# Performance work log

Hardware: AMD Instinct MI355X
Metric: run time of the kernel (lower is better)

## Reference

```python
import jax, jax.numpy as jnp
import numpy as np

HIDDEN = 2048
N_HEADS = 16
Q_DIM = N_HEADS * 128  # 2048
INTER = 10944
EPS = 1e-6
B, S = 2, 2048


def rms_norm(x, w, eps):
    var = jnp.mean(jnp.square(x), axis=-1, keepdims=True)
    return x * jax.lax.rsqrt(var + eps) * w


def setup_inputs() -> dict:
    key = jax.random.key(0)
    ks = jax.random.split(key, 8)
    x = jax.random.normal(ks[0], (B, S, HIDDEN), dtype=jnp.float32)
    positions = jnp.broadcast_to(jnp.arange(S, dtype=jnp.int32), (B, S))
    sc = 0.02
    return {
        "x": x,
        "positions": positions,
        "in_w": jnp.ones((HIDDEN,), dtype=jnp.float32),
        "post_w": jnp.ones((HIDDEN,), dtype=jnp.float32),
        "Wq": jax.random.normal(ks[1], (Q_DIM, HIDDEN), dtype=jnp.float32) * sc,
        "Wo": jax.random.normal(ks[2], (HIDDEN, Q_DIM), dtype=jnp.float32) * sc,
        "Wg": jax.random.normal(ks[3], (INTER, HIDDEN), dtype=jnp.float32) * sc,
        "Wu": jax.random.normal(ks[4], (INTER, HIDDEN), dtype=jnp.float32) * sc,
        "Wd": jax.random.normal(ks[5], (HIDDEN, INTER), dtype=jnp.float32) * sc,
    }


def reference(x, positions, in_w, post_w, Wq, Wo, Wg, Wu, Wd):
    b, s, h = x.shape
    xf = x.reshape(-1, h)                       # [T, H]
    h_norm = rms_norm(xf, in_w, EPS)            # RMSNorm (input_layernorm)
    q = jnp.einsum('th,qh->tq', h_norm, Wq)     # q_proj
    hidden = xf + jnp.einsum('tq,hq->th', q, Wo)  # o_proj + residual
    h_post = rms_norm(hidden, post_w, EPS)      # post_attention_layernorm
    gate = jax.nn.silu(jnp.einsum('th,ih->ti', h_post, Wg))
    up = jnp.einsum('th,ih->ti', h_post, Wu)
    mlp = jnp.einsum('ti,hi->th', gate * up, Wd)  # down_proj
    return (hidden + mlp).reshape(b, s, h)
```

## Files before the change

### kernel.cpp

```cpp
#include <hip/hip_runtime.h>
#include <hip/hip_bf16.h>
#include <stdint.h>


typedef __bf16 bf16;
typedef bf16 bf16x8 __attribute__((ext_vector_type(8)));
typedef bf16 bf16x4 __attribute__((ext_vector_type(4)));
typedef float f32x4 __attribute__((ext_vector_type(4)));

#define HID     2048
#define TOK     4096
#define INTER   10944
#define INTER_P 11008
#define BK      32

__device__ __forceinline__ void gload_lds16(const bf16* g, bf16* l) {
    __builtin_amdgcn_global_load_lds(
        (const __attribute__((address_space(1))) void*)g,
        (__attribute__((address_space(3))) void*)l, 16, 0, 0);
}

__global__ __launch_bounds__(256) void conv_pad(const float* __restrict__ src,
                                                bf16* __restrict__ dst,
                                                int n_src, int n_dst) {
    int i = (blockIdx.x * 256 + threadIdx.x) * 4;
    if (i >= n_dst) return;
    float4 v = make_float4(0.f, 0.f, 0.f, 0.f);
    if (i < n_src) v = *(const float4*)(src + i);
    bf16x4 o;
    o[0] = (bf16)v.x; o[1] = (bf16)v.y; o[2] = (bf16)v.z; o[3] = (bf16)v.w;
    *(bf16x4*)(dst + i) = o;
}

__global__ __launch_bounds__(256) void conv_wd(const float* __restrict__ src,
                                               bf16* __restrict__ dst) {
    int i = (blockIdx.x * 256 + threadIdx.x) * 4;
    if (i >= HID * INTER_P) return;
    int row = i / INTER_P;
    int col = i - row * INTER_P;
    float4 v = make_float4(0.f, 0.f, 0.f, 0.f);
    if (col < INTER)
        v = *(const float4*)(src + (size_t)row * INTER + col);
    bf16x4 o;
    o[0] = (bf16)v.x; o[1] = (bf16)v.y; o[2] = (bf16)v.z; o[3] = (bf16)v.w;
    *(bf16x4*)(dst + i) = o;
}

__global__ __launch_bounds__(256) void rmsnorm_k(const float* __restrict__ x,
                                                 const float* __restrict__ w,
                                                 bf16* __restrict__ out) {
    const int row = blockIdx.x;
    const int tid = threadIdx.x;
    const float* xr = x + (size_t)row * HID + tid * 8;
    float4 v0 = *(const float4*)(xr);
    float4 v1 = *(const float4*)(xr + 4);
    float s = v0.x * v0.x + v0.y * v0.y + v0.z * v0.z + v0.w * v0.w +
              v1.x * v1.x + v1.y * v1.y + v1.z * v1.z + v1.w * v1.w;
    #pragma unroll
    for (int o = 32; o > 0; o >>= 1) s += __shfl_down(s, o);
    __shared__ float red[4];
    if ((tid & 63) == 0) red[tid >> 6] = s;
    __syncthreads();
    float tot = red[0] + red[1] + red[2] + red[3];
    float scale = rsqrtf(tot * (1.0f / (float)HID) + 1e-6f);
    float4 w0 = *(const float4*)(w + tid * 8);
    float4 w1 = *(const float4*)(w + tid * 8 + 4);
    bf16x8 o8;
    o8[0] = (bf16)(v0.x * scale * w0.x);
    o8[1] = (bf16)(v0.y * scale * w0.y);
    o8[2] = (bf16)(v0.z * scale * w0.z);
    o8[3] = (bf16)(v0.w * scale * w0.w);
    o8[4] = (bf16)(v1.x * scale * w1.x);
    o8[5] = (bf16)(v1.y * scale * w1.y);
    o8[6] = (bf16)(v1.z * scale * w1.z);
    o8[7] = (bf16)(v1.w * scale * w1.w);
    *(bf16x8*)(out + (size_t)row * HID + tid * 8) = o8;
}

template <int EPI>
__global__ __launch_bounds__(512, 4) void gemm_bt5(const bf16* __restrict__ A,
                                                   const bf16* __restrict__ W,
                                                   const float* __restrict__ res,
                                                   void* __restrict__ out,
                                                   int N, int K) {
    __shared__ bf16 lA[128 * BK];
    __shared__ bf16 lW[128 * BK];
    const int tid = threadIdx.x;
    const int rowBase = blockIdx.x * 128;
    const int colBase = blockIdx.y * 128;
    const int wave = tid >> 6, lane = tid & 63;
    const int wm = (wave >> 2) * 64, wn = (wave & 3) * 32;
    const int lr = lane & 15, kq = lane >> 4;

    f32x4 acc[4][2] = {};
    const bf16* Ab = A + (size_t)rowBase * K;
    const bf16* Wb = W + (size_t)colBase * K;

    const int sr = tid >> 2;
    const int ss = (tid & 3) ^ ((sr >> 1) & 3);
    const size_t goff = (size_t)sr * K + ss * 8;

    int aoff[4], woff[2];
    #pragma unroll
    for (int i = 0; i < 4; ++i) {
        int r = wm + i * 16 + lr;
        aoff[i] = r * BK + (kq ^ ((r >> 1) & 3)) * 8;
    }
    #pragma unroll
    for (int i = 0; i < 2; ++i) {
        int r = wn + i * 16 + lr;
        woff[i] = r * BK + (kq ^ ((r >> 1) & 3)) * 8;
    }

    for (int k0 = 0; k0 < K; k0 += BK) {
        gload_lds16(Ab + goff + k0, &lA[tid * 8]);
        gload_lds16(Wb + goff + k0, &lW[tid * 8]);
        __syncthreads();
        bf16x8 af[4], wf[2];
        #pragma unroll
        for (int i = 0; i < 4; ++i) af[i] = *(const bf16x8*)&lA[aoff[i]];
        #pragma unroll
        for (int i = 0; i < 2; ++i) wf[i] = *(const bf16x8*)&lW[woff[i]];
        #pragma unroll
        for (int mi = 0; mi < 4; ++mi)
            #pragma unroll
            for (int ni = 0; ni < 2; ++ni)
                acc[mi][ni] = __builtin_amdgcn_mfma_f32_16x16x32_bf16(
                    af[mi], wf[ni], acc[mi][ni], 0, 0, 0);
        __syncthreads();
    }
    const int rq = lane >> 4, cn = lane & 15;
    #pragma unroll
    for (int mi = 0; mi < 4; ++mi) {
        #pragma unroll
        for (int ni = 0; ni < 2; ++ni) {
            int col = colBase + wn + ni * 16 + cn;
            #pragma unroll
            for (int r = 0; r < 4; ++r) {
                int row = rowBase + wm + mi * 16 + rq * 4 + r;
                size_t idx = (size_t)row * N + col;
                float v = acc[mi][ni][r];
                if (EPI == 0) ((bf16*)out)[idx] = (bf16)v;
                else          ((float*)out)[idx] = res[idx] + v;
            }
        }
    }
}

__global__ __launch_bounds__(512, 4) void gemm_gu5(const bf16* __restrict__ A,
                                                   const bf16* __restrict__ Wg,
                                                   const bf16* __restrict__ Wu,
                                                   bf16* __restrict__ out,
                                                   int N, int K) {
    __shared__ bf16 lA[128 * BK];
    __shared__ bf16 lG[128 * BK];
    __shared__ bf16 lU[128 * BK];
    const int tid = threadIdx.x;
    const int rowBase = blockIdx.x * 128;
    const int colBase = blockIdx.y * 128;
    const int wave = tid >> 6, lane = tid & 63;
    const int wm = (wave >> 2) * 64, wn = (wave & 3) * 32;
    const int lr = lane & 15, kq = lane >> 4;

    f32x4 ag[4][2] = {};
    f32x4 au[4][2] = {};
    const bf16* Ab = A + (size_t)rowBase * K;
    const bf16* Gb = Wg + (size_t)colBase * K;
    const bf16* Ub = Wu + (size_t)colBase * K;

    const int sr = tid >> 2;
    const int ss = (tid & 3) ^ ((sr >> 1) & 3);
    const size_t goff = (size_t)sr * K + ss * 8;

    int aoff[4], boff[2];
    #pragma unroll
    for (int i = 0; i < 4; ++i) {
        int r = wm + i * 16 + lr;
        aoff[i] = r * BK + (kq ^ ((r >> 1) & 3)) * 8;
    }
    #pragma unroll
    for (int i = 0; i < 2; ++i) {
        int r = wn + i * 16 + lr;
        boff[i] = r * BK + (kq ^ ((r >> 1) & 3)) * 8;
    }

    for (int k0 = 0; k0 < K; k0 += BK) {
        gload_lds16(Ab + goff + k0, &lA[tid * 8]);
        gload_lds16(Gb + goff + k0, &lG[tid * 8]);
        gload_lds16(Ub + goff + k0, &lU[tid * 8]);
        __syncthreads();
        bf16x8 af[4], gf[2], uf[2];
        #pragma unroll
        for (int i = 0; i < 4; ++i) af[i] = *(const bf16x8*)&lA[aoff[i]];
        #pragma unroll
        for (int i = 0; i < 2; ++i) {
            gf[i] = *(const bf16x8*)&lG[boff[i]];
            uf[i] = *(const bf16x8*)&lU[boff[i]];
        }
        #pragma unroll
        for (int mi = 0; mi < 4; ++mi)
            #pragma unroll
            for (int ni = 0; ni < 2; ++ni) {
                ag[mi][ni] = __builtin_amdgcn_mfma_f32_16x16x32_bf16(
                    af[mi], gf[ni], ag[mi][ni], 0, 0, 0);
                au[mi][ni] = __builtin_amdgcn_mfma_f32_16x16x32_bf16(
                    af[mi], uf[ni], au[mi][ni], 0, 0, 0);
            }
        __syncthreads();
    }
    const int rq = lane >> 4, cn = lane & 15;
    #pragma unroll
    for (int mi = 0; mi < 4; ++mi) {
        #pragma unroll
        for (int ni = 0; ni < 2; ++ni) {
            int col = colBase + wn + ni * 16 + cn;
            #pragma unroll
            for (int r = 0; r < 4; ++r) {
                int row = rowBase + wm + mi * 16 + rq * 4 + r;
                float g = ag[mi][ni][r];
                float u = au[mi][ni][r];
                float sg = g / (1.0f + __expf(-g));
                out[(size_t)row * N + col] = (bf16)(sg * u);
            }
        }
    }
}

extern "C" void kernel_launch(void* const* d_in, const int* in_sizes, int n_in,
                              void* d_out, int out_size, void* d_ws, size_t ws_size,
                              hipStream_t stream) {
    const float* x      = (const float*)d_in[0];
    const float* in_w   = (const float*)d_in[2];
    const float* post_w = (const float*)d_in[3];
    const float* Wq     = (const float*)d_in[4];
    const float* Wo     = (const float*)d_in[5];
    const float* Wg     = (const float*)d_in[6];
    const float* Wu     = (const float*)d_in[7];
    const float* Wd     = (const float*)d_in[8];

    char* ws = (char*)d_ws;
    bf16*  X    = (bf16*)(ws + 0);
    bf16*  Yq   = (bf16*)(ws + 16777216);
    float* hid  = (float*)(ws + 33554432);
    bf16*  gu   = (bf16*)(ws + 67108864);
    bf16*  w0   = (bf16*)(ws + 157286400);
    bf16*  w1   = (bf16*)(ws + 202375168);
    bf16*  wsm  = (bf16*)(ws + 247463936);

    const int nGU  = INTER_P * HID;
    const int nGUs = INTER * HID;
    const int nSq  = HID * HID;

    conv_pad<<<nGU / 4 / 256, 256, 0, stream>>>(Wg, w0, nGUs, nGU);
    conv_pad<<<nGU / 4 / 256, 256, 0, stream>>>(Wu, w1, nGUs, nGU);
    conv_pad<<<nSq / 4 / 256, 256, 0, stream>>>(Wq, wsm, nSq, nSq);

    rmsnorm_k<<<TOK, 256, 0, stream>>>(x, in_w, X);
    gemm_bt5<0><<<dim3(TOK / 128, HID / 128), 512, 0, stream>>>(
        X, wsm, nullptr, Yq, HID, HID);
    conv_pad<<<nSq / 4 / 256, 256, 0, stream>>>(Wo, wsm, nSq, nSq);
    gemm_bt5<1><<<dim3(TOK / 128, HID / 128), 512, 0, stream>>>(
        Yq, wsm, x, hid, HID, HID);
    rmsnorm_k<<<TOK, 256, 0, stream>>>(hid, post_w, X);
    gemm_gu5<<<dim3(TOK / 128, INTER_P / 128), 512, 0, stream>>>(
        X, w0, w1, gu, INTER_P, HID);
    conv_wd<<<nGU / 4 / 256, 256, 0, stream>>>(Wd, w0);
    gemm_bt5<1><<<dim3(TOK / 128, HID / 128), 512, 0, stream>>>(
        gu, w0, hid, (float*)d_out, HID, INTER_P);
}
```

Baseline: 1.093 ms.

## Rewrite GEMMs with 256x128 tiles and multi-stage async LDS pipelining

Replaces the single-buffered 128x128 GEMM kernels with 256-row tiles whose K loop runs through a 3-stage (projections/down) or 4-stage (gate/up) ring of LDS buffers. Global-to-LDS loads for future K steps are interleaved between MFMA phases, with vmcnt waits, raw barriers and setprio hints. The goal is to hide global memory latency and raise arithmetic intensity per block. In exchange it uses much more LDS and registers per block, which lowers occupancy, and the hand-written barrier and waitcnt scheme is fragile.

```diff
diff --git a/kernel.cpp b/kernel.cpp
--- a/kernel.cpp
+++ b/kernel.cpp
@@ -12,13 +12,16 @@
 #define TOK     4096
 #define INTER   10944
 #define INTER_P 11008
-#define BK      32
 
 __device__ __forceinline__ void gload_lds16(const bf16* g, bf16* l) {
     __builtin_amdgcn_global_load_lds(
         (const __attribute__((address_space(1))) void*)g,
         (__attribute__((address_space(3))) void*)l, 16, 0, 0);
 }
+
+#define SBAR()      asm volatile("s_barrier" ::: "memory")
+#define WAIT_BAR(n) asm volatile("s_waitcnt vmcnt(" #n ")\n\ts_barrier" ::: "memory")
+#define FMA16(d, a, b) d = __builtin_amdgcn_mfma_f32_16x16x32_bf16(a, b, d, 0, 0, 0)
 
 __global__ __launch_bounds__(256) void conv_pad(const float* __restrict__ src,
                                                 bf16* __restrict__ dst,
@@ -77,153 +80,273 @@
     *(bf16x8*)(out + (size_t)row * HID + tid * 8) = o8;
 }
 
+#define ABUF2 16384
+#define WBUF2 8192
+#define BUFE2 24576
+
+#define STGA(b, kk, i) gload_lds16(sA[i] + (kk), &lds[(b) * BUFE2 + (i) * 4096 + ldst])
+#define STGW(b, kk, j) gload_lds16(sW[j] + (kk), &lds[(b) * BUFE2 + ABUF2 + (j) * 4096 + ldst])
+
 template <int EPI>
-__global__ __launch_bounds__(512, 4) void gemm_bt5(const bf16* __restrict__ A,
-                                                   const bf16* __restrict__ W,
-                                                   const float* __restrict__ res,
-                                                   void* __restrict__ out,
-                                                   int N, int K) {
-    __shared__ bf16 lA[128 * BK];
-    __shared__ bf16 lW[128 * BK];
+__global__ __launch_bounds__(512, 2) void gemm_p2(const bf16* __restrict__ A,
+                                                  const bf16* __restrict__ W,
+                                                  const float* __restrict__ res,
+                                                  void* __restrict__ out,
+                                                  int N, int K) {
+    extern __shared__ bf16 lds[];
     const int tid = threadIdx.x;
-    const int rowBase = blockIdx.x * 128;
+    const int rowBase = blockIdx.x * 256;
     const int colBase = blockIdx.y * 128;
     const int wave = tid >> 6, lane = tid & 63;
-    const int wm = (wave >> 2) * 64, wn = (wave & 3) * 32;
-    const int lr = lane & 15, kq = lane >> 4;
-
-    f32x4 acc[4][2] = {};
-    const bf16* Ab = A + (size_t)rowBase * K;
-    const bf16* Wb = W + (size_t)colBase * K;
-
-    const int sr = tid >> 2;
-    const int ss = (tid & 3) ^ ((sr >> 1) & 3);
-    const size_t goff = (size_t)sr * K + ss * 8;
-
-    int aoff[4], woff[2];
-    #pragma unroll
-    for (int i = 0; i < 4; ++i) {
-        int r = wm + i * 16 + lr;
-        aoff[i] = r * BK + (kq ^ ((r >> 1) & 3)) * 8;
-    }
-    #pragma unroll
-    for (int i = 0; i < 2; ++i) {
-        int r = wn + i * 16 + lr;
-        woff[i] = r * BK + (kq ^ ((r >> 1) & 3)) * 8;
-    }
-
-    for (int k0 = 0; k0 < K; k0 += BK) {
-        gload_lds16(Ab + goff + k0, &lA[tid * 8]);
-        gload_lds16(Wb + goff + k0, &lW[tid * 8]);
-        __syncthreads();
-        bf16x8 af[4], wf[2];
-        #pragma unroll
-        for (int i = 0; i < 4; ++i) af[i] = *(const bf16x8*)&lA[aoff[i]];
-        #pragma unroll
-        for (int i = 0; i < 2; ++i) wf[i] = *(const bf16x8*)&lW[woff[i]];
-        #pragma unroll
-        for (int mi = 0; mi < 4; ++mi)
+    const int wm = wave >> 1, wn = wave & 1;
+    const int fr = lane & 15, kq = lane >> 4;
+
+    const int slr = tid >> 3;
+    const int sc  = (tid & 7) ^ (slr & 7);
+    const bf16* sA[4];
+    #pragma unroll
+    for (int i = 0; i < 4; ++i)
+        sA[i] = A + (size_t)(rowBase + i * 64 + slr) * K + sc * 8;
+    const bf16* sW[2];
+    #pragma unroll
+    for (int j = 0; j < 2; ++j)
+        sW[j] = W + (size_t)(colBase + j * 64 + slr) * K + sc * 8;
+    const int ldst = tid * 8;
+
+    int aof[2][2][2], wof[2][2][2];
+    #pragma unroll
+    for (int q = 0; q < 2; ++q)
+      #pragma unroll
+      for (int ii = 0; ii < 2; ++ii) {
+        const int ra = wm * 64 + q * 32 + ii * 16 + fr;
+        const int rw = wn * 64 + q * 32 + ii * 16 + fr;
+        #pragma unroll
+        for (int ks = 0; ks < 2; ++ks) {
+            aof[q][ii][ks] = ra * 64 + (((ks * 4 + kq) ^ (ra & 7)) * 8);
+            wof[q][ii][ks] = ABUF2 + rw * 64 + (((ks * 4 + kq) ^ (rw & 7)) * 8);
+        }
+      }
+
+    f32x4 acc[4][4] = {};
+    bf16x8 af[2][2], w0[2][2], w1[2][2];
+    const int NT = K >> 6;
+
+    STGA(0, 0, 0); STGA(0, 0, 1); STGA(0, 0, 2); STGA(0, 0, 3);
+    STGW(0, 0, 0); STGW(0, 0, 1);
+    STGA(1, 64, 0); STGA(1, 64, 1); STGA(1, 64, 2); STGA(1, 64, 3);
+    STGW(1, 64, 0); STGW(1, 64, 1);
+    WAIT_BAR(6);
+
+    int buf = 0, sbuf = 2;
+    for (int t = 0; t < NT; ++t) {
+        const int bb = buf * BUFE2;
+        const bool st = (t + 2) < NT;
+        const int kk = (t + 2) << 6;
+        if (st) { STGA(sbuf, kk, 0); STGA(sbuf, kk, 1); }
+        #pragma unroll
+        for (int ii = 0; ii < 2; ++ii)
+          #pragma unroll
+          for (int ks = 0; ks < 2; ++ks) {
+            af[ii][ks] = *(const bf16x8*)&lds[bb + aof[0][ii][ks]];
+            w0[ii][ks] = *(const bf16x8*)&lds[bb + wof[0][ii][ks]];
+          }
+        SBAR();
+        __builtin_amdgcn_s_setprio(1);
+        #pragma unroll
+        for (int ks = 0; ks < 2; ++ks)
+          #pragma unroll
+          for (int ii = 0; ii < 2; ++ii)
             #pragma unroll
-            for (int ni = 0; ni < 2; ++ni)
-                acc[mi][ni] = __builtin_amdgcn_mfma_f32_16x16x32_bf16(
-                    af[mi], wf[ni], acc[mi][ni], 0, 0, 0);
-        __syncthreads();
+            for (int jj = 0; jj < 2; ++jj)
+                FMA16(acc[ii][jj], af[ii][ks], w0[jj][ks]);
+        __builtin_amdgcn_s_setprio(0);
+        SBAR();
+        if (st) { STGA(sbuf, kk, 2); STGA(sbuf, kk, 3); }
+        #pragma unroll
+        for (int jj = 0; jj < 2; ++jj)
+          #pragma unroll
+          for (int ks = 0; ks < 2; ++ks)
+            w1[jj][ks] = *(const bf16x8*)&lds[bb + wof[1][jj][ks]];
+        SBAR();
+        __builtin_amdgcn_s_setprio(1);
+        #pragma unroll
+        for (int ks = 0; ks < 2; ++ks)
+          #pragma unroll
+          for (int ii = 0; ii < 2; ++ii)
+            #pragma unroll
+            for (int jj = 0; jj < 2; ++jj)
+                FMA16(acc[ii][2 + jj], af[ii][ks], w1[jj][ks]);
+        __builtin_amdgcn_s_setprio(0);
+        SBAR();
+        if (st) STGW(sbuf, kk, 0);
+        #pragma unroll
+        for (int ii = 0; ii < 2; ++ii)
+          #pragma unroll
+          for (int ks = 0; ks < 2; ++ks)
+            af[ii][ks] = *(const bf16x8*)&lds[bb + aof[1][ii][ks]];
+        SBAR();
+        __builtin_amdgcn_s_setprio(1);
+        #pragma unroll
+        for (int ks = 0; ks < 2; ++ks)
+          #pragma unroll
+          for (int ii = 0; ii < 2; ++ii)
+            #pragma unroll
+            for (int jj = 0; jj < 2; ++jj)
+                FMA16(acc[2 + ii][2 + jj], af[ii][ks], w1[jj][ks]);
+        __builtin_amdgcn_s_setprio(0);
+        SBAR();
+        if (st) STGW(sbuf, kk, 1);
+        SBAR();
+        __builtin_amdgcn_s_setprio(1);
+        #pragma unroll
+        for (int ks = 0; ks < 2; ++ks)
+          #pragma unroll
+          for (int ii = 0; ii < 2; ++ii)
+            #pragma unroll
+            for (int jj = 0; jj < 2; ++jj)
+                FMA16(acc[2 + ii][jj], af[ii][ks], w0[jj][ks]);
+        __builtin_amdgcn_s_setprio(0);
+        if (st) WAIT_BAR(6); else WAIT_BAR(0);
+        buf  = (buf  == 2) ? 0 : buf + 1;
+        sbuf = (sbuf == 2) ? 0 : sbuf + 1;
     }
     const int rq = lane >> 4, cn = lane & 15;
     #pragma unroll
-    for (int mi = 0; mi < 4; ++mi) {
-        #pragma unroll
-        for (int ni = 0; ni < 2; ++ni) {
-            int col = colBase + wn + ni * 16 + cn;
-            #pragma unroll
-            for (int r = 0; r < 4; ++r) {
-                int row = rowBase + wm + mi * 16 + rq * 4 + r;
-                size_t idx = (size_t)row * N + col;
-                float v = acc[mi][ni][r];
-                if (EPI == 0) ((bf16*)out)[idx] = (bf16)v;
-                else          ((float*)out)[idx] = res[idx] + v;
-            }
-        }
-    }
-}
-
-__global__ __launch_bounds__(512, 4) void gemm_gu5(const bf16* __restrict__ A,
+    for (int mi = 0; mi < 4; ++mi)
+      #pragma unroll
+      for (int nj = 0; nj < 4; ++nj) {
+        const int col = colBase + wn * 64 + nj * 16 + cn;
+        #pragma unroll
+        for (int r = 0; r < 4; ++r) {
+            const int row = rowBase + wm * 64 + mi * 16 + rq * 4 + r;
+            const size_t idx = (size_t)row * N + col;
+            const float v = acc[mi][nj][r];
+            if (EPI == 0) ((bf16*)out)[idx] = (bf16)v;
+            else          ((float*)out)[idx] = res[idx] + v;
+        }
+      }
+}
+
+#define ABUF3 8192
+#define GBUF3 4096
+#define BUFE3 16384
+
+__global__ __launch_bounds__(512, 2) void gemm_gup(const bf16* __restrict__ A,
                                                    const bf16* __restrict__ Wg,
                                                    const bf16* __restrict__ Wu,
                                                    bf16* __restrict__ out,
                                                    int N, int K) {
-    __shared__ bf16 lA[128 * BK];
-    __shared__ bf16 lG[128 * BK];
-    __shared__ bf16 lU[128 * BK];
+    extern __shared__ bf16 lds[];
     const int tid = threadIdx.x;
-    const int rowBase = blockIdx.x * 128;
+    const int rowBase = blockIdx.x * 256;
     const int colBase = blockIdx.y * 128;
     const int wave = tid >> 6, lane = tid & 63;
-    const int wm = (wave >> 2) * 64, wn = (wave & 3) * 32;
-    const int lr = lane & 15, kq = lane >> 4;
-
-    f32x4 ag[4][2] = {};
-    f32x4 au[4][2] = {};
-    const bf16* Ab = A + (size_t)rowBase * K;
-    const bf16* Gb = Wg + (size_t)colBase * K;
-    const bf16* Ub = Wu + (size_t)colBase * K;
-
-    const int sr = tid >> 2;
-    const int ss = (tid & 3) ^ ((sr >> 1) & 3);
-    const size_t goff = (size_t)sr * K + ss * 8;
-
-    int aoff[4], boff[2];
-    #pragma unroll
-    for (int i = 0; i < 4; ++i) {
-        int r = wm + i * 16 + lr;
-        aoff[i] = r * BK + (kq ^ ((r >> 1) & 3)) * 8;
+    const int wm = wave >> 1, wn = wave & 1;
+    const int fr = lane & 15, kq = lane >> 4;
+
+    const int slr = tid >> 2;
+    const int sc  = (tid & 3) ^ ((slr >> 1) & 3);
+    const bf16* sA0 = A  + (size_t)(rowBase +       slr) * K + sc * 8;
+    const bf16* sA1 = A  + (size_t)(rowBase + 128 + slr) * K + sc * 8;
+    const bf16* sG  = Wg + (size_t)(colBase +       slr) * K + sc * 8;
+    const bf16* sU  = Wu + (size_t)(colBase +       slr) * K + sc * 8;
+    const int ldst = tid * 8;
+
+    int aof[4], gof[2][2];
+    #pragma unroll
+    for (int mi = 0; mi < 4; ++mi) {
+        const int r = wm * 64 + mi * 16 + fr;
+        aof[mi] = r * 32 + ((kq ^ ((r >> 1) & 3)) * 8);
     }
     #pragma unroll
-    for (int i = 0; i < 2; ++i) {
-        int r = wn + i * 16 + lr;
-        boff[i] = r * BK + (kq ^ ((r >> 1) & 3)) * 8;
+    for (int q = 0; q < 2; ++q)
+      #pragma unroll
+      for (int jj = 0; jj < 2; ++jj) {
+        const int r = wn * 64 + q * 32 + jj * 16 + fr;
+        gof[q][jj] = ABUF3 + r * 32 + ((kq ^ ((r >> 1) & 3)) * 8);
+      }
+
+    f32x4 ag[4][4] = {}, au[4][4] = {};
+    bf16x8 af[4], gq[2], uq[2];
+    const int NT = K >> 5;
+
+    #pragma unroll
+    for (int b = 0; b < 3; ++b) {
+        gload_lds16(sA0 + b * 32, &lds[b * BUFE3 + ldst]);
+        gload_lds16(sA1 + b * 32, &lds[b * BUFE3 + 4096 + ldst]);
+        gload_lds16(sG  + b * 32, &lds[b * BUFE3 + ABUF3 + ldst]);
+        gload_lds16(sU  + b * 32, &lds[b * BUFE3 + ABUF3 + GBUF3 + ldst]);
     }
-
-    for (int k0 = 0; k0 < K; k0 += BK) {
-        gload_lds16(Ab + goff + k0, &lA[tid * 8]);
-        gload_lds16(Gb + goff + k0, &lG[tid * 8]);
-        gload_lds16(Ub + goff + k0, &lU[tid * 8]);
-        __syncthreads();
-        bf16x8 af[4], gf[2], uf[2];
-        #pragma unroll
-        for (int i = 0; i < 4; ++i) af[i] = *(const bf16x8*)&lA[aoff[i]];
-        #pragma unroll
-        for (int i = 0; i < 2; ++i) {
-            gf[i] = *(const bf16x8*)&lG[boff[i]];
-            uf[i] = *(const bf16x8*)&lU[boff[i]];
+    WAIT_BAR(8);
+
+    int buf = 0, sbuf = 3;
+    for (int t = 0; t < NT; ++t) {
+        const int bb = buf * BUFE3;
+        const bool st = (t + 3) < NT;
+        const int kk = (t + 3) << 5;
+        if (st) {
+            gload_lds16(sA0 + kk, &lds[sbuf * BUFE3 + ldst]);
+            gload_lds16(sA1 + kk, &lds[sbuf * BUFE3 + 4096 + ldst]);
         }
         #pragma unroll
         for (int mi = 0; mi < 4; ++mi)
-            #pragma unroll
-            for (int ni = 0; ni < 2; ++ni) {
-                ag[mi][ni] = __builtin_amdgcn_mfma_f32_16x16x32_bf16(
-                    af[mi], gf[ni], ag[mi][ni], 0, 0, 0);
-                au[mi][ni] = __builtin_amdgcn_mfma_f32_16x16x32_bf16(
-                    af[mi], uf[ni], au[mi][ni], 0, 0, 0);
-            }
-        __syncthreads();
+            af[mi] = *(const bf16x8*)&lds[bb + aof[mi]];
+        #pragma unroll
+        for (int jj = 0; jj < 2; ++jj) {
+            gq[jj] = *(const bf16x8*)&lds[bb + gof[0][jj]];
+            uq[jj] = *(const bf16x8*)&lds[bb + gof[0][jj] + GBUF3];
+        }
+        SBAR();
+        __builtin_amdgcn_s_setprio(1);
+        #pragma unroll
+        for (int mi = 0; mi < 4; ++mi)
+          #pragma unroll
+          for (int jj = 0; jj < 2; ++jj) {
+            FMA16(ag[mi][jj], af[mi], gq[jj]);
+            FMA16(au[mi][jj], af[mi], uq[jj]);
+          }
+        __builtin_amdgcn_s_setprio(0);
+        SBAR();
+        if (st) {
+            gload_lds16(sG + kk, &lds[sbuf * BUFE3 + ABUF3 + ldst]);
+            gload_lds16(sU + kk, &lds[sbuf * BUFE3 + ABUF3 + GBUF3 + ldst]);
+        }
+        #pragma unroll
+        for (int jj = 0; jj < 2; ++jj) {
+            gq[jj] = *(const bf16x8*)&lds[bb + gof[1][jj]];
+            uq[jj] = *(const bf16x8*)&lds[bb + gof[1][jj] + GBUF3];
+        }
+        SBAR();
+        __builtin_amdgcn_s_setprio(1);
+        #pragma unroll
+        for (int mi = 0; mi < 4; ++mi)
+          #pragma unroll
+          for (int jj = 0; jj < 2; ++jj) {
+            FMA16(ag[mi][2 + jj], af[mi], gq[jj]);
+            FMA16(au[mi][2 + jj], af[mi], uq[jj]);
+          }
+        __builtin_amdgcn_s_setprio(0);
+        if (st)                WAIT_BAR(8);
+        else if ((t + 2) < NT) WAIT_BAR(4);
+        else                   WAIT_BAR(0);
+        buf  = (buf + 1) & 3;
+        sbuf = (sbuf + 1) & 3;
     }
     const int rq = lane >> 4, cn = lane & 15;
     #pragma unroll
-    for (int mi = 0; mi < 4; ++mi) {
-        #pragma unroll
-        for (int ni = 0; ni < 2; ++ni) {
-            int col = colBase + wn + ni * 16 + cn;
-            #pragma unroll
-            for (int r = 0; r < 4; ++r) {
-                int row = rowBase + wm + mi * 16 + rq * 4 + r;
-                float g = ag[mi][ni][r];
-                float u = au[mi][ni][r];
-                float sg = g / (1.0f + __expf(-g));
-                out[(size_t)row * N + col] = (bf16)(sg * u);
-            }
-        }
-    }
+    for (int mi = 0; mi < 4; ++mi)
+      #pragma unroll
+      for (int nj = 0; nj < 4; ++nj) {
+        const int col = colBase + wn * 64 + nj * 16 + cn;
+        #pragma unroll
+        for (int r = 0; r < 4; ++r) {
+            const int row = rowBase + wm * 64 + mi * 16 + rq * 4 + r;
+            const float g = ag[mi][nj][r];
+            const float u = au[mi][nj][r];
+            const float sg = g / (1.0f + __expf(-g));
+            out[(size_t)row * N + col] = (bf16)(sg * u);
+        }
+      }
 }
 
 extern "C" void kernel_launch(void* const* d_in, const int* in_sizes, int n_in,
@@ -238,6 +361,13 @@
     const float* Wu     = (const float*)d_in[7];
     const float* Wd     = (const float*)d_in[8];
 
+    hipFuncSetAttribute(reinterpret_cast<const void*>(&gemm_p2<0>),
+                        hipFuncAttributeMaxDynamicSharedMemorySize, 3 * BUFE2 * 2);
+    hipFuncSetAttribute(reinterpret_cast<const void*>(&gemm_p2<1>),
+                        hipFuncAttributeMaxDynamicSharedMemorySize, 3 * BUFE2 * 2);
+    hipFuncSetAttribute(reinterpret_cast<const void*>(&gemm_gup),
+                        hipFuncAttributeMaxDynamicSharedMemorySize, 4 * BUFE3 * 2);
+
     char* ws = (char*)d_ws;
     bf16*  X    = (bf16*)(ws + 0);
     bf16*  Yq   = (bf16*)(ws + 16777216);
@@ -256,15 +386,15 @@
     conv_pad<<<nSq / 4 / 256, 256, 0, stream>>>(Wq, wsm, nSq, nSq);
 
     rmsnorm_k<<<TOK, 256, 0, stream>>>(x, in_w, X);
-    gemm_bt5<0><<<dim3(TOK / 128, HID / 128), 512, 0, stream>>>(
+    gemm_p2<0><<<dim3(TOK / 256, HID / 128), 512, 3 * BUFE2 * 2, stream>>>(
         X, wsm, nullptr, Yq, HID, HID);
     conv_pad<<<nSq / 4 / 256, 256, 0, stream>>>(Wo, wsm, nSq, nSq);
-    gemm_bt5<1><<<dim3(TOK / 128, HID / 128), 512, 0, stream>>>(
+    gemm_p2<1><<<dim3(TOK / 256, HID / 128), 512, 3 * BUFE2 * 2, stream>>>(
         Yq, wsm, x, hid, HID, HID);
     rmsnorm_k<<<TOK, 256, 0, stream>>>(hid, post_w, X);
-    gemm_gu5<<<dim3(TOK / 128, INTER_P / 128), 512, 0, stream>>>(
+    gemm_gup<<<dim3(TOK / 256, INTER_P / 128), 512, 4 * BUFE3 * 2, stream>>>(
         X, w0, w1, gu, INTER_P, HID);
     conv_wd<<<nGU / 4 / 256, 256, 0, stream>>>(Wd, w0);
-    gemm_bt5<1><<<dim3(TOK / 128, HID / 128), 512, 0, stream>>>(
+    gemm_p2<1><<<dim3(TOK / 256, HID / 128), 512, 3 * BUFE2 * 2, stream>>>(
         gu, w0, hid, (float*)d_out, HID, INTER_P);
 }
```

Result: faster. 967.2 us (-11.5%).
